# Kernel tuning notes

Hardware: AMD Instinct MI355X
Metric: run time of the kernel (lower is better)

## Reference

```python
import jax, jax.numpy as jnp
import numpy as np

B, N, F, IMF = 16, 64, 512, 2048
EPS = 1e-5


def _linear_params(key, out_f, in_f):
    k1, k2 = jax.random.split(key)
    w = jax.random.normal(k1, (out_f, in_f), dtype=jnp.float32) * 0.02
    b = jax.random.normal(k2, (out_f,), dtype=jnp.float32) * 0.02
    return w, b


def setup_inputs() -> dict:
    key = jax.random.key(0)
    ks = jax.random.split(key, 8)
    inp = {}
    inp["input"] = jax.random.normal(ks[0], (B, N, F), dtype=jnp.float32)
    inp["im_input"] = jax.random.normal(ks[1], (B, IMF), dtype=jnp.float32)
    inp["gmlp1_w"], inp["gmlp1_b"] = _linear_params(ks[2], F, 2 * F)
    inp["gmlp2_w"], inp["gmlp2_b"] = _linear_params(ks[3], F, F)
    inp["gmlp3_w"], inp["gmlp3_b"] = _linear_params(ks[4], F, F)
    inp["im_w"], inp["im_b"] = _linear_params(ks[5], F, IMF)
    inp["bn_gamma"] = jnp.ones((F,), dtype=jnp.float32)
    inp["bn_beta"] = jnp.zeros((F,), dtype=jnp.float32)
    inp["d1_w"], inp["d1_b"] = _linear_params(ks[6], F, 2 * F)
    inp["d2_w"], inp["d2_b"] = _linear_params(ks[7], 2, F)
    return inp


def reference(input, im_input, gmlp1_w, gmlp1_b, gmlp2_w, gmlp2_b,
              gmlp3_w, gmlp3_b, im_w, im_b, bn_gamma, bn_beta,
              d1_w, d1_b, d2_w, d2_b):
    b, n, f = input.shape
    npair = n * n
    # relation_embedding: all-pairs expand + concat (replicating the exact
    # row-major reshape semantics of the original torch code, including the
    # memory-reinterpreting view used for feature2)
    feature1 = jnp.broadcast_to(input[:, None, :, :], (b, n, n, f)).reshape(b, npair, f)
    feature2 = jnp.broadcast_to(input[:, :, :, None], (b, n, f, n)).reshape(b, npair, f)
    feature = jnp.concatenate([feature1, feature2], axis=2).reshape(-1, 2 * f)  # [b*n^2, 1024]
    h = jax.nn.relu(feature @ gmlp1_w.T + gmlp1_b)
    h = jax.nn.relu(h @ gmlp2_w.T + gmlp2_b)
    h = jax.nn.relu(h @ gmlp3_w.T + gmlp3_b)
    sent_embedding = h.reshape(b, npair, f).mean(axis=1)  # [b, 512]
    # im_embedding: Linear + BatchNorm1d (training-mode batch stats) + ReLU
    img = im_input @ im_w.T + im_b
    mu = img.mean(axis=0)
    var = jnp.mean(jnp.square(img - mu), axis=0)  # biased variance
    img = bn_gamma * (img - mu) * jax.lax.rsqrt(var + EPS) + bn_beta
    img_embedding = jax.nn.relu(img)
    # net_D
    emb = jnp.concatenate([sent_embedding, img_embedding], axis=1)  # [b, 1024]
    out = jax.nn.relu(emb @ d1_w.T + d1_b) @ d2_w.T + d2_b  # [b, 2]
    return out
```

## Files before the change

kernel.cpp:

```cpp
#include <hip/hip_runtime.h>


typedef float f32x4 __attribute__((ext_vector_type(4)));
typedef __bf16 bf16x8v __attribute__((ext_vector_type(8)));
typedef __bf16 bf16x4v __attribute__((ext_vector_type(4)));

#define WS_A1Q     0u
#define WS_W1P     2097152u
#define WS_SENT    2129920u
#define WS_Y       2162688u
#define WS_IMGEMB  2195456u
#define WS_W2BF    2228224u
#define WS_W3BF    2752512u

__global__ __launch_bounds__(256) void k_prep(
    const float* __restrict__ input, const float* __restrict__ im_input,
    const float* __restrict__ g1w, const float* __restrict__ g1b,
    const float* __restrict__ g2w, const float* __restrict__ g3w,
    const float* __restrict__ imw, const float* __restrict__ imb,
    float* __restrict__ ws)
{
  __shared__ float As[16][72];
  __shared__ float Bs[16][72];
  const int blk = blockIdx.x, t = threadIdx.x;
  float4* A1Q = (float4*)ws;
  __bf16* w1p = (__bf16*)((char*)ws + WS_W1P);
  float* sent = (float*)((char*)ws + WS_SENT);
  float* yv   = (float*)((char*)ws + WS_Y);
  __bf16* w2bf = (__bf16*)((char*)ws + WS_W2BF);
  __bf16* w3bf = (__bf16*)((char*)ws + WS_W3BF);

  if (blk < 128) {
    const int tm = blk >> 3, tn = blk & 7;
    const int m0 = tm * 64, o0 = tn * 64;
    const int ty = t >> 4, tx = t & 15;
    const int lrow = t >> 2, lk4 = (t & 3) * 4;
    float acc[4][4] = {};
    for (int kc = 0; kc < 512; kc += 16) {
      float4 av = *(const float4*)(input + (m0 + lrow) * 512 + kc + lk4);
      float4 bw = *(const float4*)(g1w + (size_t)(o0 + lrow) * 1024 + kc + lk4);
      __syncthreads();
      As[lk4 + 0][lrow] = av.x; As[lk4 + 1][lrow] = av.y;
      As[lk4 + 2][lrow] = av.z; As[lk4 + 3][lrow] = av.w;
      Bs[lk4 + 0][lrow] = bw.x; Bs[lk4 + 1][lrow] = bw.y;
      Bs[lk4 + 2][lrow] = bw.z; Bs[lk4 + 3][lrow] = bw.w;
      __syncthreads();
#pragma unroll
      for (int kk = 0; kk < 16; ++kk) {
        float a4[4], b4[4];
        *(float4*)a4 = *(const float4*)&As[kk][4 * ty];
        *(float4*)b4 = *(const float4*)&Bs[kk][4 * tx];
#pragma unroll
        for (int ii = 0; ii < 4; ++ii)
#pragma unroll
          for (int jj = 0; jj < 4; ++jj)
            acc[ii][jj] += a4[ii] * b4[jj];
      }
    }
    float4 bias = *(const float4*)(g1b + o0 + 4 * tx);
#pragma unroll
    for (int ii = 0; ii < 4; ++ii) {
      float4 v;
      v.x = acc[ii][0] + bias.x; v.y = acc[ii][1] + bias.y;
      v.z = acc[ii][2] + bias.z; v.w = acc[ii][3] + bias.w;
      A1Q[(tm * 128 + tn * 16 + tx) * 64 + 4 * ty + ii] = v;
    }
  } else if (blk < 384) {
    int idx = ((blk - 128) * 256 + t) * 8;
    const float* src; __bf16* dst; int off;
    if (idx < 262144) { src = g2w; dst = w2bf; off = idx; }
    else              { src = g3w; dst = w3bf; off = idx - 262144; }
    int o = off >> 9, k = off & 511;
    int ks = k >> 5, quad = (k >> 3) & 3;
    int doff = (o >> 4) * 8192 + ks * 512 + (quad * 16 + (o & 15)) * 8;
    float4 v0 = *(const float4*)(src + off);
    float4 v1 = *(const float4*)(src + off + 4);
    bf16x8v h;
    h[0] = (__bf16)v0.x; h[1] = (__bf16)v0.y; h[2] = (__bf16)v0.z; h[3] = (__bf16)v0.w;
    h[4] = (__bf16)v1.x; h[5] = (__bf16)v1.y; h[6] = (__bf16)v1.z; h[7] = (__bf16)v1.w;
    *(bf16x8v*)(dst + doff) = h;
  } else if (blk < 400) {
    int idx = (blk - 384) * 256 + t;
    int o = idx >> 3, s = idx & 7;
    const float* p = g1w + (size_t)o * 1024 + 512 + s * 64;
    float sum = 0.f;
#pragma unroll
    for (int u = 0; u < 64; u += 4) {
      float4 v = *(const float4*)(p + u);
      sum += v.x + v.y + v.z + v.w;
    }
    int base = (o >> 4) * 512 + (o & 15) * 8 + s;
    w1p[base]       = (__bf16)sum;
    w1p[base + 128] = (__bf16)0.f;
    w1p[base + 256] = (__bf16)0.f;
    w1p[base + 384] = (__bf16)0.f;
    sent[idx] = 0.f; sent[idx + 4096] = 0.f;
  } else {
    int o = blk - 400;
    int wv = t >> 6, l = t & 63;
    const float* wrow = imw + (size_t)o * 2048;
    for (int bb = 0; bb < 4; ++bb) {
      int b = wv * 4 + bb;
      const float* xr = im_input + (size_t)b * 2048;
      float s = 0.f;
#pragma unroll
      for (int u = 0; u < 8; ++u) {
        int k = u * 256 + l * 4;
        float4 xv = *(const float4*)(xr + k);
        float4 wx = *(const float4*)(wrow + k);
        s += xv.x * wx.x + xv.y * wx.y + xv.z * wx.z + xv.w * wx.w;
      }
#pragma unroll
      for (int m = 32; m >= 1; m >>= 1) s += __shfl_xor(s, m);
      if (l == 0) yv[b * 512 + o] = s + imb[o];
    }
  }
}

__device__ __forceinline__ void kloop(const __bf16* __restrict__ wl,
                                      const __bf16* __restrict__ hbuf,
                                      int p16, int quad, f32x4 acc[8][4])
{
  const int msk3 = (p16 & 7) << 3;
  bf16x8v a0[4], a1[4], an[4];
#pragma unroll
  for (int ot = 0; ot < 4; ++ot) a0[ot] = *(const bf16x8v*)(wl + ot * 8192);
#pragma unroll
  for (int ot = 0; ot < 4; ++ot) a1[ot] = *(const bf16x8v*)(wl + (ot + 4) * 8192);
#pragma unroll 2
  for (int ks = 0; ks < 16; ++ks) {
    const int kcb = (((ks * 4 + quad) << 3) ^ msk3);
    bf16x8v bf[4];
#pragma unroll
    for (int mt = 0; mt < 4; ++mt)
      bf[mt] = *(const bf16x8v*)(hbuf + (p16 + 16 * mt) * 512 + kcb);
    if (ks < 15) {
#pragma unroll
      for (int ot = 0; ot < 4; ++ot)
        an[ot] = *(const bf16x8v*)(wl + (ks + 1) * 512 + ot * 8192);
    }
#pragma unroll
    for (int ot = 0; ot < 4; ++ot)
#pragma unroll
      for (int mt = 0; mt < 4; ++mt)
        acc[ot][mt] = __builtin_amdgcn_mfma_f32_16x16x32_bf16(a0[ot], bf[mt], acc[ot][mt], 0, 0, 0);
#pragma unroll
    for (int ot = 0; ot < 4; ++ot)
#pragma unroll
      for (int mt = 0; mt < 4; ++mt)
        acc[4 + ot][mt] = __builtin_amdgcn_mfma_f32_16x16x32_bf16(a1[ot], bf[mt], acc[4 + ot][mt], 0, 0, 0);
    if (ks < 15) {
#pragma unroll
      for (int ot = 0; ot < 4; ++ot)
        a1[ot] = *(const bf16x8v*)(wl + (ks + 1) * 512 + (ot + 4) * 8192);
#pragma unroll
      for (int ot = 0; ot < 4; ++ot) a0[ot] = an[ot];
    }
  }
}

__global__ __launch_bounds__(256, 2) void k_main(
    const float* __restrict__ input,
    const float* __restrict__ g2b, const float* __restrict__ g3b,
    const float* __restrict__ bng, const float* __restrict__ bnb,
    float* __restrict__ ws)
{
  const int blk = blockIdx.x, t = threadIdx.x;
  const float4* A1Q = (const float4*)ws;
  const __bf16* w1p = (const __bf16*)((char*)ws + WS_W1P);
  float* sent = (float*)((char*)ws + WS_SENT);
  float* yv   = (float*)((char*)ws + WS_Y);
  float* imge = (float*)((char*)ws + WS_IMGEMB);
  const __bf16* w2bf = (const __bf16*)((char*)ws + WS_W2BF);
  const __bf16* w3bf = (const __bf16*)((char*)ws + WS_W3BF);

  if (blk == 1024) {
#pragma unroll
    for (int rep = 0; rep < 2; ++rep) {
      int o = t + rep * 256;
      float vals[16];
      float mu = 0.f;
#pragma unroll
      for (int b = 0; b < 16; ++b) { vals[b] = yv[b * 512 + o]; mu += vals[b]; }
      mu *= (1.f / 16.f);
      float var = 0.f;
#pragma unroll
      for (int b = 0; b < 16; ++b) { float d = vals[b] - mu; var += d * d; }
      var *= (1.f / 16.f);
      float sc = bng[o] * rsqrtf(var + 1e-5f);
      float sh = bnb[o] - mu * sc;
#pragma unroll
      for (int b = 0; b < 16; ++b)
        imge[b * 512 + o] = fmaxf(vals[b] * sc + sh, 0.f);
    }
    return;
  }

  __shared__ __align__(16) __bf16 hbuf[32768];

  const int b = blk >> 6, i = blk & 63;
  const int w = t >> 6, l = t & 63;
  const int quad = l >> 4, p16 = l & 15;

  float xreg[8];
  {
    const float* xr = input + (size_t)(b * 64 + i) * 512 + l * 8;
    *(float4*)xreg       = *(const float4*)xr;
    *(float4*)(xreg + 4) = *(const float4*)(xr + 4);
  }

  f32x4 acc[8][4];

  {
    bf16x8v xb[4];
#pragma unroll
    for (int mt = 0; mt < 4; ++mt) {
#pragma unroll
      for (int j = 0; j < 8; ++j) {
        float v = __shfl(xreg[j], p16 + 16 * mt);
        xb[mt][j] = (quad == 0) ? (__bf16)v : (__bf16)0.f;
      }
    }
#pragma unroll
    for (int ot = 0; ot < 8; ++ot)
#pragma unroll
      for (int mt = 0; mt < 4; ++mt) { f32x4 z = {0.f, 0.f, 0.f, 0.f}; acc[ot][mt] = z; }
#pragma unroll
    for (int ot = 0; ot < 8; ++ot) {
      bf16x8v af = *(const bf16x8v*)(w1p + (w * 8 + ot) * 512 + l * 8);
#pragma unroll
      for (int mt = 0; mt < 4; ++mt)
        acc[ot][mt] = __builtin_amdgcn_mfma_f32_16x16x32_bf16(af, xb[mt], acc[ot][mt], 0, 0, 0);
    }
    const float4* cq = A1Q + ((size_t)b * 128 + w * 32) * 64;
#pragma unroll
    for (int ot = 0; ot < 8; ++ot) {
#pragma unroll
      for (int mt = 0; mt < 4; ++mt) {
        float4 c = cq[(ot * 4 + quad) * 64 + 16 * mt + p16];
        f32x4 v = acc[ot][mt];
        bf16x4v h;
        h[0] = (__bf16)fmaxf(v[0] + c.x, 0.f);
        h[1] = (__bf16)fmaxf(v[1] + c.y, 0.f);
        h[2] = (__bf16)fmaxf(v[2] + c.z, 0.f);
        h[3] = (__bf16)fmaxf(v[3] + c.w, 0.f);
        int row = p16 + 16 * mt;
        int col = w * 128 + ot * 16 + quad * 4;
        *(bf16x4v*)(hbuf + row * 512 + (((col >> 3) ^ (row & 7)) << 3) + (col & 7)) = h;
      }
    }
  }
  __syncthreads();

#pragma unroll
  for (int ot = 0; ot < 8; ++ot)
#pragma unroll
    for (int mt = 0; mt < 4; ++mt) { f32x4 z = {0.f, 0.f, 0.f, 0.f}; acc[ot][mt] = z; }

  kloop(w2bf + (size_t)(w * 8) * 8192 + l * 8, hbuf, p16, quad, acc);
  __syncthreads();
#pragma unroll
  for (int ot = 0; ot < 8; ++ot) {
    float4 b2 = *(const float4*)(g2b + w * 128 + ot * 16 + quad * 4);
#pragma unroll
    for (int mt = 0; mt < 4; ++mt) {
      f32x4 v = acc[ot][mt];
      bf16x4v h;
      h[0] = (__bf16)fmaxf(v[0] + b2.x, 0.f);
      h[1] = (__bf16)fmaxf(v[1] + b2.y, 0.f);
      h[2] = (__bf16)fmaxf(v[2] + b2.z, 0.f);
      h[3] = (__bf16)fmaxf(v[3] + b2.w, 0.f);
      int row = p16 + 16 * mt;
      int col = w * 128 + ot * 16 + quad * 4;
      *(bf16x4v*)(hbuf + row * 512 + (((col >> 3) ^ (row & 7)) << 3) + (col & 7)) = h;
    }
  }
  __syncthreads();

#pragma unroll
  for (int ot = 0; ot < 8; ++ot)
#pragma unroll
    for (int mt = 0; mt < 4; ++mt) { f32x4 z = {0.f, 0.f, 0.f, 0.f}; acc[ot][mt] = z; }

  kloop(w3bf + (size_t)(w * 8) * 8192 + l * 8, hbuf, p16, quad, acc);

#pragma unroll
  for (int ot = 0; ot < 8; ++ot) {
    float4 b3 = *(const float4*)(g3b + w * 128 + ot * 16 + quad * 4);
    float bb[4] = {b3.x, b3.y, b3.z, b3.w};
#pragma unroll
    for (int r = 0; r < 4; ++r) {
      float s = 0.f;
#pragma unroll
      for (int mt = 0; mt < 4; ++mt) s += fmaxf(acc[ot][mt][r] + bb[r], 0.f);
      s += __shfl_xor(s, 1);
      s += __shfl_xor(s, 2);
      s += __shfl_xor(s, 4);
      s += __shfl_xor(s, 8);
      if (p16 == 0)
        atomicAdd(&sent[b * 512 + w * 128 + ot * 16 + quad * 4 + r], s * (1.0f / 4096.0f));
    }
  }
}

__global__ __launch_bounds__(128) void k_head(
    const float* __restrict__ d1w, const float* __restrict__ d1b,
    const float* __restrict__ d2w, const float* __restrict__ d2b,
    const float* __restrict__ ws, float* __restrict__ out)
{
  __shared__ float emb[1024];
  const float* sent = (const float*)((const char*)ws + WS_SENT);
  const float* imge = (const float*)((const char*)ws + WS_IMGEMB);
  const int b = blockIdx.x >> 2, sl = blockIdx.x & 3, t = threadIdx.x;
  ((float4*)emb)[t]       = ((const float4*)(sent + b * 512))[t];
  ((float4*)(emb + 512))[t] = ((const float4*)(imge + b * 512))[t];
  __syncthreads();
  const int w2 = t >> 6, l = t & 63;
  float p0 = 0.f, p1 = 0.f;
  for (int rr = 0; rr < 64; ++rr) {
    int row = sl * 128 + w2 * 64 + rr;
    const float* wr = d1w + (size_t)row * 1024 + l * 4;
    float s = 0.f;
#pragma unroll
    for (int c = 0; c < 4; ++c) {
      float4 wv = *(const float4*)(wr + c * 256);
      float4 ev = *(const float4*)(emb + l * 4 + c * 256);
      s += wv.x * ev.x + wv.y * ev.y + wv.z * ev.z + wv.w * ev.w;
    }
#pragma unroll
    for (int m = 32; m >= 1; m >>= 1) s += __shfl_xor(s, m);
    float h = fmaxf(s + d1b[row], 0.f);
    p0 += d2w[row] * h;
    p1 += d2w[512 + row] * h;
  }
  if (l == 0) {
    if (sl == 0 && w2 == 0) { p0 += d2b[0]; p1 += d2b[1]; }
    atomicAdd(&out[b * 2 + 0], p0);
    atomicAdd(&out[b * 2 + 1], p1);
  }
}

extern "C" void kernel_launch(void* const* d_in, const int* in_sizes, int n_in,
                              void* d_out, int out_size, void* d_ws, size_t ws_size,
                              hipStream_t stream)
{
  const float* input    = (const float*)d_in[0];
  const float* im_input = (const float*)d_in[1];
  const float* g1w = (const float*)d_in[2];
  const float* g1b = (const float*)d_in[3];
  const float* g2w = (const float*)d_in[4];
  const float* g2b = (const float*)d_in[5];
  const float* g3w = (const float*)d_in[6];
  const float* g3b = (const float*)d_in[7];
  const float* imw = (const float*)d_in[8];
  const float* imb = (const float*)d_in[9];
  const float* bng = (const float*)d_in[10];
  const float* bnb = (const float*)d_in[11];
  const float* d1w = (const float*)d_in[12];
  const float* d1b = (const float*)d_in[13];
  const float* d2w = (const float*)d_in[14];
  const float* d2b = (const float*)d_in[15];
  float* out = (float*)d_out;
  float* ws  = (float*)d_ws;

  hipMemsetAsync(d_out, 0, (size_t)out_size * 4, stream);
  k_prep<<<912, 256, 0, stream>>>(input, im_input, g1w, g1b, g2w, g3w, imw, imb, ws);
  k_main<<<1025, 256, 0, stream>>>(input, g2b, g3b, bng, bnb, ws);
  k_head<<<64, 128, 0, stream>>>(d1w, d1b, d2w, d2b, ws, out);
}
```

Measured before the change: 217.4 us.

## Process two i-rows per block with 8 waves to halve weight reloads

Each k_main block now handles two adjacent i rows (128 pairs) with 512 threads. Each wave owns 4 output tiles across 8 M tiles instead of 8 output tiles across 4 M tiles, so every weight fragment loaded from global memory feeds twice as many MFMAs and total weight traffic drops by half. The cost is doubled LDS use (128KB per block), which limits how many blocks fit on a CU, plus more B-fragment LDS reads per k step.

```diff
diff --git a/kernel.cpp b/kernel.cpp
--- a/kernel.cpp
+++ b/kernel.cpp
@@ -119,21 +119,23 @@
 
 __device__ __forceinline__ void kloop(const __bf16* __restrict__ wl,
                                       const __bf16* __restrict__ hbuf,
-                                      int p16, int quad, f32x4 acc[8][4])
+                                      int p16, int quad, f32x4 acc[4][8])
 {
   const int msk3 = (p16 & 7) << 3;
-  bf16x8v a0[4], a1[4], an[4];
-#pragma unroll
-  for (int ot = 0; ot < 4; ++ot) a0[ot] = *(const bf16x8v*)(wl + ot * 8192);
-#pragma unroll
-  for (int ot = 0; ot < 4; ++ot) a1[ot] = *(const bf16x8v*)(wl + (ot + 4) * 8192);
+  int moff[8];
+#pragma unroll
+  for (int mt = 0; mt < 8; ++mt)
+    moff[mt] = (mt >> 2) * 32768 + (p16 + 16 * (mt & 3)) * 512;
+  bf16x8v a[4], an[4];
+#pragma unroll
+  for (int ot = 0; ot < 4; ++ot) a[ot] = *(const bf16x8v*)(wl + ot * 8192);
 #pragma unroll 2
   for (int ks = 0; ks < 16; ++ks) {
     const int kcb = (((ks * 4 + quad) << 3) ^ msk3);
-    bf16x8v bf[4];
-#pragma unroll
-    for (int mt = 0; mt < 4; ++mt)
-      bf[mt] = *(const bf16x8v*)(hbuf + (p16 + 16 * mt) * 512 + kcb);
+    bf16x8v bf[8];
+#pragma unroll
+    for (int mt = 0; mt < 8; ++mt)
+      bf[mt] = *(const bf16x8v*)(hbuf + moff[mt] + kcb);
     if (ks < 15) {
 #pragma unroll
       for (int ot = 0; ot < 4; ++ot)
@@ -143,23 +145,20 @@
     for (int ot = 0; ot < 4; ++ot)
 #pragma unroll
       for (int mt = 0; mt < 4; ++mt)
-        acc[ot][mt] = __builtin_amdgcn_mfma_f32_16x16x32_bf16(a0[ot], bf[mt], acc[ot][mt], 0, 0, 0);
+        acc[ot][mt] = __builtin_amdgcn_mfma_f32_16x16x32_bf16(a[ot], bf[mt], acc[ot][mt], 0, 0, 0);
 #pragma unroll
     for (int ot = 0; ot < 4; ++ot)
 #pragma unroll
-      for (int mt = 0; mt < 4; ++mt)
-        acc[4 + ot][mt] = __builtin_amdgcn_mfma_f32_16x16x32_bf16(a1[ot], bf[mt], acc[4 + ot][mt], 0, 0, 0);
+      for (int mt = 4; mt < 8; ++mt)
+        acc[ot][mt] = __builtin_amdgcn_mfma_f32_16x16x32_bf16(a[ot], bf[mt], acc[ot][mt], 0, 0, 0);
     if (ks < 15) {
 #pragma unroll
-      for (int ot = 0; ot < 4; ++ot)
-        a1[ot] = *(const bf16x8v*)(wl + (ks + 1) * 512 + (ot + 4) * 8192);
-#pragma unroll
-      for (int ot = 0; ot < 4; ++ot) a0[ot] = an[ot];
-    }
-  }
-}
-
-__global__ __launch_bounds__(256, 2) void k_main(
+      for (int ot = 0; ot < 4; ++ot) a[ot] = an[ot];
+    }
+  }
+}
+
+__global__ __launch_bounds__(512, 2) void k_main(
     const float* __restrict__ input,
     const float* __restrict__ g2b, const float* __restrict__ g3b,
     const float* __restrict__ bng, const float* __restrict__ bnb,
@@ -174,131 +173,137 @@
   const __bf16* w2bf = (const __bf16*)((char*)ws + WS_W2BF);
   const __bf16* w3bf = (const __bf16*)((char*)ws + WS_W3BF);
 
-  if (blk == 1024) {
-#pragma unroll
-    for (int rep = 0; rep < 2; ++rep) {
-      int o = t + rep * 256;
-      float vals[16];
-      float mu = 0.f;
-#pragma unroll
-      for (int b = 0; b < 16; ++b) { vals[b] = yv[b * 512 + o]; mu += vals[b]; }
-      mu *= (1.f / 16.f);
-      float var = 0.f;
-#pragma unroll
-      for (int b = 0; b < 16; ++b) { float d = vals[b] - mu; var += d * d; }
-      var *= (1.f / 16.f);
-      float sc = bng[o] * rsqrtf(var + 1e-5f);
-      float sh = bnb[o] - mu * sc;
-#pragma unroll
-      for (int b = 0; b < 16; ++b)
-        imge[b * 512 + o] = fmaxf(vals[b] * sc + sh, 0.f);
-    }
+  if (blk == 512) {
+    int o = t;
+    float vals[16];
+    float mu = 0.f;
+#pragma unroll
+    for (int b = 0; b < 16; ++b) { vals[b] = yv[b * 512 + o]; mu += vals[b]; }
+    mu *= (1.f / 16.f);
+    float var = 0.f;
+#pragma unroll
+    for (int b = 0; b < 16; ++b) { float d = vals[b] - mu; var += d * d; }
+    var *= (1.f / 16.f);
+    float sc = bng[o] * rsqrtf(var + 1e-5f);
+    float sh = bnb[o] - mu * sc;
+#pragma unroll
+    for (int b = 0; b < 16; ++b)
+      imge[b * 512 + o] = fmaxf(vals[b] * sc + sh, 0.f);
     return;
   }
 
-  __shared__ __align__(16) __bf16 hbuf[32768];
-
-  const int b = blk >> 6, i = blk & 63;
+  __shared__ __align__(16) __bf16 hbuf[65536];
+
+  const int b = blk >> 5, ipair = blk & 31;
   const int w = t >> 6, l = t & 63;
   const int quad = l >> 4, p16 = l & 15;
 
-  float xreg[8];
+  float xreg0[8], xreg1[8];
   {
-    const float* xr = input + (size_t)(b * 64 + i) * 512 + l * 8;
-    *(float4*)xreg       = *(const float4*)xr;
-    *(float4*)(xreg + 4) = *(const float4*)(xr + 4);
-  }
-
-  f32x4 acc[8][4];
+    const float* xr0 = input + (size_t)(b * 64 + ipair * 2) * 512 + l * 8;
+    *(float4*)xreg0       = *(const float4*)xr0;
+    *(float4*)(xreg0 + 4) = *(const float4*)(xr0 + 4);
+    *(float4*)xreg1       = *(const float4*)(xr0 + 512);
+    *(float4*)(xreg1 + 4) = *(const float4*)(xr0 + 516);
+  }
+
+  f32x4 acc[4][8];
 
   {
-    bf16x8v xb[4];
+    bf16x8v xb[8];
 #pragma unroll
     for (int mt = 0; mt < 4; ++mt) {
 #pragma unroll
       for (int j = 0; j < 8; ++j) {
-        float v = __shfl(xreg[j], p16 + 16 * mt);
-        xb[mt][j] = (quad == 0) ? (__bf16)v : (__bf16)0.f;
+        float v0 = __shfl(xreg0[j], p16 + 16 * mt);
+        float v1 = __shfl(xreg1[j], p16 + 16 * mt);
+        xb[mt][j]     = (quad == 0) ? (__bf16)v0 : (__bf16)0.f;
+        xb[mt + 4][j] = (quad == 0) ? (__bf16)v1 : (__bf16)0.f;
       }
     }
 #pragma unroll
-    for (int ot = 0; ot < 8; ++ot)
-#pragma unroll
-      for (int mt = 0; mt < 4; ++mt) { f32x4 z = {0.f, 0.f, 0.f, 0.f}; acc[ot][mt] = z; }
-#pragma unroll
-    for (int ot = 0; ot < 8; ++ot) {
-      bf16x8v af = *(const bf16x8v*)(w1p + (w * 8 + ot) * 512 + l * 8);
-#pragma unroll
-      for (int mt = 0; mt < 4; ++mt)
+    for (int ot = 0; ot < 4; ++ot)
+#pragma unroll
+      for (int mt = 0; mt < 8; ++mt) { f32x4 z = {0.f, 0.f, 0.f, 0.f}; acc[ot][mt] = z; }
+#pragma unroll
+    for (int ot = 0; ot < 4; ++ot) {
+      bf16x8v af = *(const bf16x8v*)(w1p + (w * 4 + ot) * 512 + l * 8);
+#pragma unroll
+      for (int mt = 0; mt < 8; ++mt)
         acc[ot][mt] = __builtin_amdgcn_mfma_f32_16x16x32_bf16(af, xb[mt], acc[ot][mt], 0, 0, 0);
     }
-    const float4* cq = A1Q + ((size_t)b * 128 + w * 32) * 64;
-#pragma unroll
-    for (int ot = 0; ot < 8; ++ot) {
-#pragma unroll
-      for (int mt = 0; mt < 4; ++mt) {
-        float4 c = cq[(ot * 4 + quad) * 64 + 16 * mt + p16];
-        f32x4 v = acc[ot][mt];
-        bf16x4v h;
-        h[0] = (__bf16)fmaxf(v[0] + c.x, 0.f);
-        h[1] = (__bf16)fmaxf(v[1] + c.y, 0.f);
-        h[2] = (__bf16)fmaxf(v[2] + c.z, 0.f);
-        h[3] = (__bf16)fmaxf(v[3] + c.w, 0.f);
-        int row = p16 + 16 * mt;
-        int col = w * 128 + ot * 16 + quad * 4;
-        *(bf16x4v*)(hbuf + row * 512 + (((col >> 3) ^ (row & 7)) << 3) + (col & 7)) = h;
+    const float4* cq = A1Q + ((size_t)b * 128 + w * 16) * 64;
+#pragma unroll
+    for (int ot = 0; ot < 4; ++ot) {
+#pragma unroll
+      for (int mtp = 0; mtp < 4; ++mtp) {
+        float4 c = cq[(ot * 4 + quad) * 64 + 16 * mtp + p16];
+        int row = p16 + 16 * mtp;
+        int col = w * 64 + ot * 16 + quad * 4;
+        int addr = row * 512 + (((col >> 3) ^ (row & 7)) << 3) + (col & 7);
+#pragma unroll
+        for (int tau = 0; tau < 2; ++tau) {
+          f32x4 v = acc[ot][tau * 4 + mtp];
+          bf16x4v h;
+          h[0] = (__bf16)fmaxf(v[0] + c.x, 0.f);
+          h[1] = (__bf16)fmaxf(v[1] + c.y, 0.f);
+          h[2] = (__bf16)fmaxf(v[2] + c.z, 0.f);
+          h[3] = (__bf16)fmaxf(v[3] + c.w, 0.f);
+          *(bf16x4v*)(hbuf + tau * 32768 + addr) = h;
+        }
       }
     }
   }
   __syncthreads();
 
 #pragma unroll
-  for (int ot = 0; ot < 8; ++ot)
-#pragma unroll
-    for (int mt = 0; mt < 4; ++mt) { f32x4 z = {0.f, 0.f, 0.f, 0.f}; acc[ot][mt] = z; }
-
-  kloop(w2bf + (size_t)(w * 8) * 8192 + l * 8, hbuf, p16, quad, acc);
+  for (int ot = 0; ot < 4; ++ot)
+#pragma unroll
+    for (int mt = 0; mt < 8; ++mt) { f32x4 z = {0.f, 0.f, 0.f, 0.f}; acc[ot][mt] = z; }
+
+  kloop(w2bf + (size_t)(w * 4) * 8192 + l * 8, hbuf, p16, quad, acc);
   __syncthreads();
 #pragma unroll
-  for (int ot = 0; ot < 8; ++ot) {
-    float4 b2 = *(const float4*)(g2b + w * 128 + ot * 16 + quad * 4);
-#pragma unroll
-    for (int mt = 0; mt < 4; ++mt) {
+  for (int ot = 0; ot < 4; ++ot) {
+    float4 b2 = *(const float4*)(g2b + w * 64 + ot * 16 + quad * 4);
+#pragma unroll
+    for (int mt = 0; mt < 8; ++mt) {
       f32x4 v = acc[ot][mt];
       bf16x4v h;
       h[0] = (__bf16)fmaxf(v[0] + b2.x, 0.f);
       h[1] = (__bf16)fmaxf(v[1] + b2.y, 0.f);
       h[2] = (__bf16)fmaxf(v[2] + b2.z, 0.f);
       h[3] = (__bf16)fmaxf(v[3] + b2.w, 0.f);
-      int row = p16 + 16 * mt;
-      int col = w * 128 + ot * 16 + quad * 4;
-      *(bf16x4v*)(hbuf + row * 512 + (((col >> 3) ^ (row & 7)) << 3) + (col & 7)) = h;
+      int row = p16 + 16 * (mt & 3);
+      int col = w * 64 + ot * 16 + quad * 4;
+      *(bf16x4v*)(hbuf + (mt >> 2) * 32768 + row * 512 +
+                  (((col >> 3) ^ (row & 7)) << 3) + (col & 7)) = h;
     }
   }
   __syncthreads();
 
 #pragma unroll
-  for (int ot = 0; ot < 8; ++ot)
-#pragma unroll
-    for (int mt = 0; mt < 4; ++mt) { f32x4 z = {0.f, 0.f, 0.f, 0.f}; acc[ot][mt] = z; }
-
-  kloop(w3bf + (size_t)(w * 8) * 8192 + l * 8, hbuf, p16, quad, acc);
-
-#pragma unroll
-  for (int ot = 0; ot < 8; ++ot) {
-    float4 b3 = *(const float4*)(g3b + w * 128 + ot * 16 + quad * 4);
+  for (int ot = 0; ot < 4; ++ot)
+#pragma unroll
+    for (int mt = 0; mt < 8; ++mt) { f32x4 z = {0.f, 0.f, 0.f, 0.f}; acc[ot][mt] = z; }
+
+  kloop(w3bf + (size_t)(w * 4) * 8192 + l * 8, hbuf, p16, quad, acc);
+
+#pragma unroll
+  for (int ot = 0; ot < 4; ++ot) {
+    float4 b3 = *(const float4*)(g3b + w * 64 + ot * 16 + quad * 4);
     float bb[4] = {b3.x, b3.y, b3.z, b3.w};
 #pragma unroll
     for (int r = 0; r < 4; ++r) {
       float s = 0.f;
 #pragma unroll
-      for (int mt = 0; mt < 4; ++mt) s += fmaxf(acc[ot][mt][r] + bb[r], 0.f);
+      for (int mt = 0; mt < 8; ++mt) s += fmaxf(acc[ot][mt][r] + bb[r], 0.f);
       s += __shfl_xor(s, 1);
       s += __shfl_xor(s, 2);
       s += __shfl_xor(s, 4);
       s += __shfl_xor(s, 8);
       if (p16 == 0)
-        atomicAdd(&sent[b * 512 + w * 128 + ot * 16 + quad * 4 + r], s * (1.0f / 4096.0f));
+        atomicAdd(&sent[b * 512 + w * 64 + ot * 16 + quad * 4 + r], s * (1.0f / 4096.0f));
     }
   }
 }
@@ -365,6 +370,6 @@
 
   hipMemsetAsync(d_out, 0, (size_t)out_size * 4, stream);
   k_prep<<<912, 256, 0, stream>>>(input, im_input, g1w, g1b, g2w, g3w, imw, imb, ws);
-  k_main<<<1025, 256, 0, stream>>>(input, g2b, g3b, bng, bnb, ws);
+  k_main<<<513, 512, 0, stream>>>(input, g2b, g3b, bng, bnb, ws);
   k_head<<<64, 128, 0, stream>>>(d1w, d1b, d2w, d2b, ws, out);
 }
```

Result: faster. 201.0 us (-7.6%).

## Process two query rows per 512-thread block and reduce head in-block

Applied to the files above, without the earlier changes.

k_main now runs 512-thread blocks that each handle two i-rows, giving each half its own 64 KB-per-block LDS region, and halves the grid. The intent is to share weight fetches (W2/W3 bf16) between the two halves through cache locality and to reduce block count. k_head moves to one 512-thread block per batch with a shared-memory reduction and direct stores, which removes the output memset and the atomics. Risks: 128 KB of LDS per block with launch_bounds(512,2) may cap occupancy at one block per CU, and the larger __syncthreads barriers cover more waves.

```diff
diff --git a/kernel.cpp b/kernel.cpp
--- a/kernel.cpp
+++ b/kernel.cpp
@@ -118,7 +118,7 @@
 }
 
 __device__ __forceinline__ void kloop(const __bf16* __restrict__ wl,
-                                      const __bf16* __restrict__ hbuf,
+                                      const __bf16* __restrict__ hb,
                                       int p16, int quad, f32x4 acc[8][4])
 {
   const int msk3 = (p16 & 7) << 3;
@@ -133,7 +133,7 @@
     bf16x8v bf[4];
 #pragma unroll
     for (int mt = 0; mt < 4; ++mt)
-      bf[mt] = *(const bf16x8v*)(hbuf + (p16 + 16 * mt) * 512 + kcb);
+      bf[mt] = *(const bf16x8v*)(hb + (p16 + 16 * mt) * 512 + kcb);
     if (ks < 15) {
 #pragma unroll
       for (int ot = 0; ot < 4; ++ot)
@@ -159,7 +159,7 @@
   }
 }
 
-__global__ __launch_bounds__(256, 2) void k_main(
+__global__ __launch_bounds__(512, 2) void k_main(
     const float* __restrict__ input,
     const float* __restrict__ g2b, const float* __restrict__ g3b,
     const float* __restrict__ bng, const float* __restrict__ bnb,
@@ -174,37 +174,36 @@
   const __bf16* w2bf = (const __bf16*)((char*)ws + WS_W2BF);
   const __bf16* w3bf = (const __bf16*)((char*)ws + WS_W3BF);
 
-  if (blk == 1024) {
-#pragma unroll
-    for (int rep = 0; rep < 2; ++rep) {
-      int o = t + rep * 256;
-      float vals[16];
-      float mu = 0.f;
-#pragma unroll
-      for (int b = 0; b < 16; ++b) { vals[b] = yv[b * 512 + o]; mu += vals[b]; }
-      mu *= (1.f / 16.f);
-      float var = 0.f;
-#pragma unroll
-      for (int b = 0; b < 16; ++b) { float d = vals[b] - mu; var += d * d; }
-      var *= (1.f / 16.f);
-      float sc = bng[o] * rsqrtf(var + 1e-5f);
-      float sh = bnb[o] - mu * sc;
-#pragma unroll
-      for (int b = 0; b < 16; ++b)
-        imge[b * 512 + o] = fmaxf(vals[b] * sc + sh, 0.f);
-    }
+  if (blk == 512) {
+    int o = t;
+    float vals[16];
+    float mu = 0.f;
+#pragma unroll
+    for (int b = 0; b < 16; ++b) { vals[b] = yv[b * 512 + o]; mu += vals[b]; }
+    mu *= (1.f / 16.f);
+    float var = 0.f;
+#pragma unroll
+    for (int b = 0; b < 16; ++b) { float d = vals[b] - mu; var += d * d; }
+    var *= (1.f / 16.f);
+    float sc = bng[o] * rsqrtf(var + 1e-5f);
+    float sh = bnb[o] - mu * sc;
+#pragma unroll
+    for (int b = 0; b < 16; ++b)
+      imge[b * 512 + o] = fmaxf(vals[b] * sc + sh, 0.f);
     return;
   }
 
-  __shared__ __align__(16) __bf16 hbuf[32768];
-
-  const int b = blk >> 6, i = blk & 63;
+  __shared__ __align__(16) __bf16 hbuf[65536];
+
+  const int b = blk >> 5, ipair = blk & 31;
   const int w = t >> 6, l = t & 63;
+  const int tau = w >> 2, wq = w & 3;
   const int quad = l >> 4, p16 = l & 15;
+  __bf16* hb = hbuf + tau * 32768;
 
   float xreg[8];
   {
-    const float* xr = input + (size_t)(b * 64 + i) * 512 + l * 8;
+    const float* xr = input + (size_t)(b * 64 + ipair * 2 + tau) * 512 + l * 8;
     *(float4*)xreg       = *(const float4*)xr;
     *(float4*)(xreg + 4) = *(const float4*)(xr + 4);
   }
@@ -227,12 +226,12 @@
       for (int mt = 0; mt < 4; ++mt) { f32x4 z = {0.f, 0.f, 0.f, 0.f}; acc[ot][mt] = z; }
 #pragma unroll
     for (int ot = 0; ot < 8; ++ot) {
-      bf16x8v af = *(const bf16x8v*)(w1p + (w * 8 + ot) * 512 + l * 8);
+      bf16x8v af = *(const bf16x8v*)(w1p + (wq * 8 + ot) * 512 + l * 8);
 #pragma unroll
       for (int mt = 0; mt < 4; ++mt)
         acc[ot][mt] = __builtin_amdgcn_mfma_f32_16x16x32_bf16(af, xb[mt], acc[ot][mt], 0, 0, 0);
     }
-    const float4* cq = A1Q + ((size_t)b * 128 + w * 32) * 64;
+    const float4* cq = A1Q + ((size_t)b * 128 + wq * 32) * 64;
 #pragma unroll
     for (int ot = 0; ot < 8; ++ot) {
 #pragma unroll
@@ -245,8 +244,8 @@
         h[2] = (__bf16)fmaxf(v[2] + c.z, 0.f);
         h[3] = (__bf16)fmaxf(v[3] + c.w, 0.f);
         int row = p16 + 16 * mt;
-        int col = w * 128 + ot * 16 + quad * 4;
-        *(bf16x4v*)(hbuf + row * 512 + (((col >> 3) ^ (row & 7)) << 3) + (col & 7)) = h;
+        int col = wq * 128 + ot * 16 + quad * 4;
+        *(bf16x4v*)(hb + row * 512 + (((col >> 3) ^ (row & 7)) << 3) + (col & 7)) = h;
       }
     }
   }
@@ -257,11 +256,11 @@
 #pragma unroll
     for (int mt = 0; mt < 4; ++mt) { f32x4 z = {0.f, 0.f, 0.f, 0.f}; acc[ot][mt] = z; }
 
-  kloop(w2bf + (size_t)(w * 8) * 8192 + l * 8, hbuf, p16, quad, acc);
+  kloop(w2bf + (size_t)(wq * 8) * 8192 + l * 8, hb, p16, quad, acc);
   __syncthreads();
 #pragma unroll
   for (int ot = 0; ot < 8; ++ot) {
-    float4 b2 = *(const float4*)(g2b + w * 128 + ot * 16 + quad * 4);
+    float4 b2 = *(const float4*)(g2b + wq * 128 + ot * 16 + quad * 4);
 #pragma unroll
     for (int mt = 0; mt < 4; ++mt) {
       f32x4 v = acc[ot][mt];
@@ -271,8 +270,8 @@
       h[2] = (__bf16)fmaxf(v[2] + b2.z, 0.f);
       h[3] = (__bf16)fmaxf(v[3] + b2.w, 0.f);
       int row = p16 + 16 * mt;
-      int col = w * 128 + ot * 16 + quad * 4;
-      *(bf16x4v*)(hbuf + row * 512 + (((col >> 3) ^ (row & 7)) << 3) + (col & 7)) = h;
+      int col = wq * 128 + ot * 16 + quad * 4;
+      *(bf16x4v*)(hb + row * 512 + (((col >> 3) ^ (row & 7)) << 3) + (col & 7)) = h;
     }
   }
   __syncthreads();
@@ -282,11 +281,11 @@
 #pragma unroll
     for (int mt = 0; mt < 4; ++mt) { f32x4 z = {0.f, 0.f, 0.f, 0.f}; acc[ot][mt] = z; }
 
-  kloop(w3bf + (size_t)(w * 8) * 8192 + l * 8, hbuf, p16, quad, acc);
+  kloop(w3bf + (size_t)(wq * 8) * 8192 + l * 8, hb, p16, quad, acc);
 
 #pragma unroll
   for (int ot = 0; ot < 8; ++ot) {
-    float4 b3 = *(const float4*)(g3b + w * 128 + ot * 16 + quad * 4);
+    float4 b3 = *(const float4*)(g3b + wq * 128 + ot * 16 + quad * 4);
     float bb[4] = {b3.x, b3.y, b3.z, b3.w};
 #pragma unroll
     for (int r = 0; r < 4; ++r) {
@@ -298,27 +297,28 @@
       s += __shfl_xor(s, 4);
       s += __shfl_xor(s, 8);
       if (p16 == 0)
-        atomicAdd(&sent[b * 512 + w * 128 + ot * 16 + quad * 4 + r], s * (1.0f / 4096.0f));
-    }
-  }
-}
-
-__global__ __launch_bounds__(128) void k_head(
+        atomicAdd(&sent[b * 512 + wq * 128 + ot * 16 + quad * 4 + r], s * (1.0f / 4096.0f));
+    }
+  }
+}
+
+__global__ __launch_bounds__(512) void k_head(
     const float* __restrict__ d1w, const float* __restrict__ d1b,
     const float* __restrict__ d2w, const float* __restrict__ d2b,
     const float* __restrict__ ws, float* __restrict__ out)
 {
   __shared__ float emb[1024];
+  __shared__ float red[8][2];
   const float* sent = (const float*)((const char*)ws + WS_SENT);
   const float* imge = (const float*)((const char*)ws + WS_IMGEMB);
-  const int b = blockIdx.x >> 2, sl = blockIdx.x & 3, t = threadIdx.x;
-  ((float4*)emb)[t]       = ((const float4*)(sent + b * 512))[t];
-  ((float4*)(emb + 512))[t] = ((const float4*)(imge + b * 512))[t];
-  __syncthreads();
-  const int w2 = t >> 6, l = t & 63;
+  const int b = blockIdx.x, t = threadIdx.x;
+  emb[t]       = sent[b * 512 + t];
+  emb[512 + t] = imge[b * 512 + t];
+  __syncthreads();
+  const int v = t >> 6, l = t & 63;
   float p0 = 0.f, p1 = 0.f;
   for (int rr = 0; rr < 64; ++rr) {
-    int row = sl * 128 + w2 * 64 + rr;
+    int row = v * 64 + rr;
     const float* wr = d1w + (size_t)row * 1024 + l * 4;
     float s = 0.f;
 #pragma unroll
@@ -333,10 +333,14 @@
     p0 += d2w[row] * h;
     p1 += d2w[512 + row] * h;
   }
-  if (l == 0) {
-    if (sl == 0 && w2 == 0) { p0 += d2b[0]; p1 += d2b[1]; }
-    atomicAdd(&out[b * 2 + 0], p0);
-    atomicAdd(&out[b * 2 + 1], p1);
+  if (l == 0) { red[v][0] = p0; red[v][1] = p1; }
+  __syncthreads();
+  if (t == 0) {
+    float q0 = d2b[0], q1 = d2b[1];
+#pragma unroll
+    for (int u = 0; u < 8; ++u) { q0 += red[u][0]; q1 += red[u][1]; }
+    out[b * 2 + 0] = q0;
+    out[b * 2 + 1] = q1;
   }
 }
 
@@ -363,8 +367,7 @@
   float* out = (float*)d_out;
   float* ws  = (float*)d_ws;
 
-  hipMemsetAsync(d_out, 0, (size_t)out_size * 4, stream);
   k_prep<<<912, 256, 0, stream>>>(input, im_input, g1w, g1b, g2w, g3w, imw, imb, ws);
-  k_main<<<1025, 256, 0, stream>>>(input, g2b, g3b, bng, bnb, ws);
-  k_head<<<64, 128, 0, stream>>>(d1w, d1b, d2w, d2b, ws, out);
-}
+  k_main<<<513, 512, 0, stream>>>(input, g2b, g3b, bng, bnb, ws);
+  k_head<<<16, 512, 0, stream>>>(d1w, d1b, d2w, d2b, ws, out);
+}
```

Result: no change. 215.4 us (-0.9%).
